# Performance work log

Hardware: AMD Instinct MI355X
Metric: run time of the kernel (lower is better)

## Reference

```python
import jax, jax.numpy as jnp
import numpy as np

N = 100000      # nodes
E = 1600000     # edges
H = 4           # num_heads
D = 16          # hidden_size per head
F_IN = 128      # input_size
HD = H * D
EPS = 1e-5


def setup_inputs() -> dict:
    key = jax.random.key(0)
    ks = jax.random.split(key, 12)
    s = 1.0 / np.sqrt(F_IN)
    feature = jax.random.normal(ks[0], (N, F_IN), jnp.float32)
    src = jax.random.randint(ks[1], (E,), 0, N, jnp.int32)
    dst = jax.random.randint(ks[2], (E,), 0, N, jnp.int32)
    Wq = jax.random.normal(ks[3], (F_IN, HD), jnp.float32) * s
    bq = jnp.zeros((HD,), jnp.float32)
    Wk = jax.random.normal(ks[4], (F_IN, HD), jnp.float32) * s
    bk = jnp.zeros((HD,), jnp.float32)
    Wv = jax.random.normal(ks[5], (F_IN, HD), jnp.float32) * s
    bv = jnp.zeros((HD,), jnp.float32)
    Wskip = jax.random.normal(ks[6], (F_IN, HD), jnp.float32) * s
    bskip = jnp.zeros((HD,), jnp.float32)
    ln_g = jnp.ones((HD,), jnp.float32)
    ln_b = jnp.zeros((HD,), jnp.float32)
    return dict(feature=feature, src=src, dst=dst, Wq=Wq, bq=bq, Wk=Wk, bk=bk,
                Wv=Wv, bv=bv, Wskip=Wskip, bskip=bskip, ln_g=ln_g, ln_b=ln_b)


def reference(feature, src, dst, Wq, bq, Wk, bk, Wv, bv, Wskip, bskip, ln_g, ln_b):
    # QKV projections, [N, H, D]; q scaled by 1/sqrt(D) (as in send_recv)
    q = ((feature @ Wq) + bq).reshape(N, H, D) * (1.0 / np.sqrt(D))
    k = ((feature @ Wk) + bk).reshape(N, H, D)
    v = ((feature @ Wv) + bv).reshape(N, H, D)
    # edge scores: sum over head dim of q[dst] * k[src] -> [E, H]
    alpha = jnp.sum(q[dst] * k[src], axis=-1)
    # segment softmax over incoming edges of each destination node
    m = jax.ops.segment_max(alpha, dst, num_segments=N)          # [N, H]
    ex = jnp.exp(alpha - m[dst])                                 # [E, H]
    z = jax.ops.segment_sum(ex, dst, num_segments=N)             # [N, H]
    a = ex / z[dst]                                              # [E, H]
    # weighted values, concat heads, scatter-sum to destination nodes
    msg = (v[src] * a[:, :, None]).reshape(E, HD)                # [E, H*D]
    out = jax.ops.segment_sum(msg, dst, num_segments=N)          # [N, H*D]
    # skip connection (no gate)
    out = out + (feature @ Wskip) + bskip
    # layer norm over last dim
    mu = jnp.mean(out, axis=-1, keepdims=True)
    var = jnp.mean(jnp.square(out - mu), axis=-1, keepdims=True)
    out = (out - mu) * jax.lax.rsqrt(var + EPS) * ln_g + ln_b
    return out
```

## Files before the change

kernel.cpp:

```cpp
#include <hip/hip_runtime.h>

typedef unsigned short u16;
typedef __attribute__((ext_vector_type(8))) short short8;
typedef __attribute__((ext_vector_type(4))) float f32x4;

#define N_NODES 100000
#define N_EDGES 1600000
#define F_IN    128
#define HD      64
#define LN_EPS  1e-5f

#define HIST_BLOCKS  6250
#define PROJ_BLOCKS  1563
#define SCAT_BLOCKS  6250
#define SCAN_BLOCKS  98

__device__ u16 g_WT[4 * HD * F_IN];

__device__ __forceinline__ float bf2f(u16 u) {
    union { unsigned int i; float f; } x;
    x.i = ((unsigned int)u) << 16;
    return x.f;
}
__device__ __forceinline__ u16 f2bf(float f) {
    unsigned int u;
    __builtin_memcpy(&u, &f, 4);
    unsigned int r = u + 0x7FFFu + ((u >> 16) & 1u);
    return (u16)(r >> 16);
}
__device__ __forceinline__ void ld4m(const void* p, int idx, int mode, float o[4]) {
    if (mode) {
        const float4 v = *reinterpret_cast<const float4*>((const float*)p + idx);
        o[0] = v.x; o[1] = v.y; o[2] = v.z; o[3] = v.w;
    } else {
        const ushort4 v = *reinterpret_cast<const ushort4*>((const u16*)p + idx);
        o[0] = bf2f(v.x); o[1] = bf2f(v.y); o[2] = bf2f(v.z); o[3] = bf2f(v.w);
    }
}

__global__ __launch_bounds__(256) void fused1_r13(
    const int* __restrict__ dst, int* __restrict__ deg,
    const void* __restrict__ Wq, const void* __restrict__ Wk,
    const void* __restrict__ Wv, const void* __restrict__ Ws,
    const u16* __restrict__ feat, int* __restrict__ mode)
{
    const int bid = blockIdx.x;
    if (bid < 16) {
        const int m  = bid >> 2;
        const int kg = bid & 3;
        const u16* W = (const u16*)((m == 0) ? Wq : (m == 1) ? Wk
                                  : (m == 2) ? Wv : Ws);
        const int t  = threadIdx.x;
        const int k  = kg * 32 + (t >> 3);
        const int c0 = (t & 7) * 8;
        union { uint4 v; u16 s[8]; } row;
        row.v = *reinterpret_cast<const uint4*>(W + k * HD + c0);
        u16* outp = g_WT + m * HD * F_IN;
        #pragma unroll
        for (int j = 0; j < 8; ++j)
            outp[(c0 + j) * F_IN + k] = row.s[j];
    } else if (bid == 16) {
        const int lane = threadIdx.x;
        if (lane < 64) {
            float mx = 0.f;
            #pragma unroll
            for (int i = 0; i < 4; ++i)
                mx = fmaxf(mx, fabsf(bf2f(feat[lane * 4 + i])));
            #pragma unroll
            for (int o = 1; o < 64; o <<= 1) mx = fmaxf(mx, __shfl_xor(mx, o));
            if (lane == 0) *mode = (mx > 1000.f) ? 1 : 0;
        }
    } else {
        const int e = (bid - 17) * 256 + threadIdx.x;
        if (e < N_EDGES) atomicAdd(&deg[dst[e]], 1);
    }
}

__global__ __launch_bounds__(1024) void scanA_r13(const int* __restrict__ deg,
                                                  int* __restrict__ off,
                                                  int* __restrict__ bsum)
{
    __shared__ int wsum[16];
    __shared__ int wexcl[16];
    const int tid = threadIdx.x, lane = tid & 63, wid = tid >> 6;
    const int idx = blockIdx.x * 1024 + tid;
    const int v = (idx < N_NODES) ? deg[idx] : 0;
    int sc = v;
    #pragma unroll
    for (int o = 1; o < 64; o <<= 1) {
        int t = __shfl_up(sc, o);
        if (lane >= o) sc += t;
    }
    if (lane == 63) wsum[wid] = sc;
    __syncthreads();
    if (tid == 0) {
        int run = 0;
        for (int i = 0; i < 16; ++i) { wexcl[i] = run; run += wsum[i]; }
        bsum[blockIdx.x] = run;
    }
    __syncthreads();
    if (idx < N_NODES) off[idx] = wexcl[wid] + (sc - v);
}

__global__ __launch_bounds__(1024) void scanC_r13(const int* __restrict__ deg,
                                                  int* __restrict__ off,
                                                  int* __restrict__ woff,
                                                  const int* __restrict__ bsum)
{
    __shared__ int base_s;
    const int tid = threadIdx.x;
    const int bid = blockIdx.x;
    if (tid == 0) {
        int run = 0;
        for (int i = 0; i < bid; ++i) run += bsum[i];
        base_s = run;
    }
    __syncthreads();
    const int base = base_s;
    const int idx = bid * 1024 + tid;
    if (idx < N_NODES) {
        const int e = off[idx] + base;
        off[idx]  = e;
        woff[idx] = e;
        if (idx == N_NODES - 1) off[N_NODES] = e + deg[idx];
    }
}

__global__ __launch_bounds__(256) void fused2_r13(
    const void* __restrict__ feature,
    const void* __restrict__ Wq, const void* __restrict__ bq,
    const void* __restrict__ Wk, const void* __restrict__ bk,
    const void* __restrict__ Wv, const void* __restrict__ bv,
    const void* __restrict__ Ws, const void* __restrict__ bs,
    u16* __restrict__ Qb, unsigned int* __restrict__ KV, u16* __restrict__ Sb,
    const int* __restrict__ mode_p,
    const int* __restrict__ src, const int* __restrict__ dst,
    int* __restrict__ woff, int* __restrict__ srcs)
{
    __shared__ u16 lq[16 * 64];
    __shared__ u16 lk[16 * 64];
    __shared__ u16 lv[16 * 64];
    __shared__ u16 ls[16 * 64];

    const int bid = blockIdx.x;

    if (bid % 5 != 0) {
        const int sid = bid - bid / 5 - 1;
        const int e = sid * 256 + threadIdx.x;
        if (e < N_EDGES) {
            const int d = dst[e];
            const int pos = atomicAdd(&woff[d], 1);
            srcs[pos] = src[e];
        }
        return;
    }

    const int pid  = bid / 5;
    const int mode = *mode_p;
    const int tid  = threadIdx.x;
    const int w    = tid >> 6;
    const int lane = tid & 63;

    const void* W;
    const void* b;
    float scale = 1.0f;
    if      (w == 0) { W = Wq; b = bq; scale = 0.25f; }
    else if (w == 1) { W = Wk; b = bk; }
    else if (w == 2) { W = Wv; b = bv; }
    else             { W = Ws; b = bs; }

    if (mode == 0) {
        const u16* F = (const u16*)feature;
        const int h = lane >> 4;
        const int c = lane & 15;

        const u16* WT = g_WT + w * HD * F_IN;
        short8 wfrag[4][4];
        #pragma unroll
        for (int ct = 0; ct < 4; ++ct) {
            const int col = ct * 16 + c;
            #pragma unroll
            for (int ks = 0; ks < 4; ++ks)
                wfrag[ct][ks] = *reinterpret_cast<const short8*>(
                    WT + col * F_IN + ks * 32 + h * 8);
        }

        float bias_f[4][4];
        #pragma unroll
        for (int ct = 0; ct < 4; ++ct) {
            const ushort4 bu =
                *reinterpret_cast<const ushort4*>((const u16*)b + ct * 16 + h * 4);
            bias_f[ct][0] = bf2f(bu.x); bias_f[ct][1] = bf2f(bu.y);
            bias_f[ct][2] = bf2f(bu.z); bias_f[ct][3] = bf2f(bu.w);
        }

        u16* Lmine = (w == 0) ? lq : (w == 1) ? lk : (w == 2) ? lv : ls;

        short8 fr[2][4];
        {
            const size_t arow = (size_t)(pid * 64 + c) * F_IN;
            #pragma unroll
            for (int ks = 0; ks < 4; ++ks)
                fr[0][ks] = *reinterpret_cast<const short8*>(F + arow + ks * 32 + h * 8);
        }

        #pragma unroll
        for (int t = 0; t < 4; ++t) {
            const int nbase = pid * 64 + t * 16;
            if (nbase >= N_NODES) break;
            const int cur = t & 1, nxt = cur ^ 1;

            const int nb2 = nbase + 16;
            if (t < 3 && nb2 < N_NODES) {
                const size_t arow = (size_t)(nb2 + c) * F_IN;
                #pragma unroll
                for (int ks = 0; ks < 4; ++ks)
                    fr[nxt][ks] =
                        *reinterpret_cast<const short8*>(F + arow + ks * 32 + h * 8);
            }

            f32x4 acc[4];
            #pragma unroll
            for (int ct = 0; ct < 4; ++ct) acc[ct] = (f32x4){0.f, 0.f, 0.f, 0.f};
            #pragma unroll
            for (int ks = 0; ks < 4; ++ks)
                #pragma unroll
                for (int ct = 0; ct < 4; ++ct)
                    acc[ct] = __builtin_amdgcn_mfma_f32_16x16x32_bf16(
                        wfrag[ct][ks], fr[cur][ks], acc[ct], 0, 0, 0);

            #pragma unroll
            for (int ct = 0; ct < 4; ++ct) {
                ushort4 pk;
                pk.x = f2bf((acc[ct][0] + bias_f[ct][0]) * scale);
                pk.y = f2bf((acc[ct][1] + bias_f[ct][1]) * scale);
                pk.z = f2bf((acc[ct][2] + bias_f[ct][2]) * scale);
                pk.w = f2bf((acc[ct][3] + bias_f[ct][3]) * scale);
                const int bo = (ct * 32 + h * 8) ^ ((c & 7) << 4);
                *reinterpret_cast<ushort4*>(
                    reinterpret_cast<char*>(Lmine) + c * 128 + bo) = pk;
            }
            __syncthreads();

            {
                const int half = tid >> 7;
                const int tt   = tid & 127;
                const int row  = tt >> 3, seg = tt & 7;
                const int ro   = (seg * 16) ^ ((row & 7) << 4);
                const uint4 qs = *reinterpret_cast<const uint4*>(
                    reinterpret_cast<const char*>(half ? ls : lq) + row * 128 + ro);
                *reinterpret_cast<uint4*>(
                    (half ? Sb : Qb) + (size_t)(nbase + row) * HD + seg * 8) = qs;

                const int krow = tid >> 4, c4 = tid & 15;
                const int ko   = (c4 * 8) ^ ((krow & 7) << 4);
                const ushort4 kk = *reinterpret_cast<const ushort4*>(
                    reinterpret_cast<const char*>(lk) + krow * 128 + ko);
                const ushort4 vv = *reinterpret_cast<const ushort4*>(
                    reinterpret_cast<const char*>(lv) + krow * 128 + ko);
                uint4 o;
                o.x = (unsigned)kk.x | ((unsigned)vv.x << 16);
                o.y = (unsigned)kk.y | ((unsigned)vv.y << 16);
                o.z = (unsigned)kk.z | ((unsigned)vv.z << 16);
                o.w = (unsigned)kk.w | ((unsigned)vv.w << 16);
                *reinterpret_cast<uint4*>(
                    KV + (size_t)(nbase + krow) * HD + c4 * 4) = o;
            }
            __syncthreads();
        }
    } else {
        const int colg  = lane & 15;
        const int nodeg = lane >> 4;
        const int c0    = colg * 4;
        const int kvsub = (w == 1) ? 0 : 1;
        u16* KVu = (u16*)KV;

        for (int st = 0; st < 4; ++st) {
            if (pid * 64 + st * 16 >= N_NODES) break;
            const int node_base = pid * 64 + st * 16 + nodeg * 4;

            float acc[4][4];
            #pragma unroll
            for (int n = 0; n < 4; ++n)
                #pragma unroll
                for (int cc = 0; cc < 4; ++cc) acc[n][cc] = 0.f;

            for (int k = 0; k < F_IN; k += 4) {
                float wv4[4][4];
                #pragma unroll
                for (int kk = 0; kk < 4; ++kk)
                    ld4m(W, (k + kk) * HD + c0, 1, wv4[kk]);
                #pragma unroll
                for (int n = 0; n < 4; ++n) {
                    float f[4];
                    ld4m(feature, (node_base + n) * F_IN + k, 1, f);
                    #pragma unroll
                    for (int cc = 0; cc < 4; ++cc)
                        acc[n][cc] += f[0] * wv4[0][cc] + f[1] * wv4[1][cc]
                                    + f[2] * wv4[2][cc] + f[3] * wv4[3][cc];
                }
            }

            float bias[4];
            ld4m(b, c0, 1, bias);

            #pragma unroll
            for (int n = 0; n < 4; ++n) {
                const int node = node_base + n;
                u16 r[4];
                #pragma unroll
                for (int cc = 0; cc < 4; ++cc)
                    r[cc] = f2bf((acc[n][cc] + bias[cc]) * scale);

                if (w == 0 || w == 3) {
                    u16* O = (w == 0) ? Qb : Sb;
                    ushort4 u4; u4.x = r[0]; u4.y = r[1]; u4.z = r[2]; u4.w = r[3];
                    *reinterpret_cast<ushort4*>(O + (size_t)node * HD + c0) = u4;
                } else {
                    #pragma unroll
                    for (int cc = 0; cc < 4; ++cc)
                        KVu[(size_t)node * 2 * HD + 2 * (c0 + cc) + kvsub] = r[cc];
                }
            }
        }
    }
}

__global__ __launch_bounds__(256) void attn_r13(
    const u16* __restrict__ Qb, const unsigned int* __restrict__ KV,
    const u16* __restrict__ Sb,
    const int* __restrict__ off, const int* __restrict__ srcs,
    const void* __restrict__ ln_g, const void* __restrict__ ln_b,
    void* __restrict__ out, const int* __restrict__ mode_p)
{
    const int mode = *mode_p;
    const int node = blockIdx.x * 4 + (threadIdx.x >> 6);
    const int lane = threadIdx.x & 63;

    const float qv = bf2f(Qb[(size_t)node * HD + lane]);
    const int e0 = off[node], e1 = off[node + 1];

    float z = 0.f, acc = 0.f;
    for (int base = e0; base < e1; base += 64) {
        const int n_e = min(64, e1 - base);
        int sidx = (base + lane < e1) ? srcs[base + lane] : 0;
        sidx = (sidx < 0) ? 0 : ((sidx >= N_NODES) ? N_NODES - 1 : sidx);
        int i = 0;
        for (; i + 4 <= n_e; i += 4) {
            const int s0 = __shfl(sidx, i);
            const int s1 = __shfl(sidx, i + 1);
            const int s2 = __shfl(sidx, i + 2);
            const int s3 = __shfl(sidx, i + 3);
            const unsigned int kv0 = KV[(size_t)s0 * HD + lane];
            const unsigned int kv1 = KV[(size_t)s1 * HD + lane];
            const unsigned int kv2 = KV[(size_t)s2 * HD + lane];
            const unsigned int kv3 = KV[(size_t)s3 * HD + lane];
            float p0 = qv * bf2f((u16)(kv0 & 0xffffu));
            float p1 = qv * bf2f((u16)(kv1 & 0xffffu));
            float p2 = qv * bf2f((u16)(kv2 & 0xffffu));
            float p3 = qv * bf2f((u16)(kv3 & 0xffffu));
            #pragma unroll
            for (int m = 1; m < 16; m <<= 1) {
                p0 += __shfl_xor(p0, m);
                p1 += __shfl_xor(p1, m);
                p2 += __shfl_xor(p2, m);
                p3 += __shfl_xor(p3, m);
            }
            const float x0 = __expf(p0);
            const float x1 = __expf(p1);
            const float x2 = __expf(p2);
            const float x3 = __expf(p3);
            z   += (x0 + x1) + (x2 + x3);
            acc += x0 * bf2f((u16)(kv0 >> 16)) + x1 * bf2f((u16)(kv1 >> 16))
                 + x2 * bf2f((u16)(kv2 >> 16)) + x3 * bf2f((u16)(kv3 >> 16));
        }
        for (; i < n_e; ++i) {
            const int s = __shfl(sidx, i);
            const unsigned int kv = KV[(size_t)s * HD + lane];
            float p = qv * bf2f((u16)(kv & 0xffffu));
            #pragma unroll
            for (int m = 1; m < 16; m <<= 1) p += __shfl_xor(p, m);
            const float ex = __expf(p);
            z   += ex;
            acc += ex * bf2f((u16)(kv >> 16));
        }
    }

    const float msg = (e1 > e0) ? (acc / z) : 0.f;
    float t = msg + bf2f(Sb[(size_t)node * HD + lane]);

    float mu = t;
    #pragma unroll
    for (int m = 1; m < 64; m <<= 1) mu += __shfl_xor(mu, m);
    mu *= (1.f / 64.f);
    const float d = t - mu;
    float var = d * d;
    #pragma unroll
    for (int m = 1; m < 64; m <<= 1) var += __shfl_xor(var, m);
    var *= (1.f / 64.f);
    const float r = d * rsqrtf(var + LN_EPS);

    const float g  = mode ? ((const float*)ln_g)[lane] : bf2f(((const u16*)ln_g)[lane]);
    const float bb = mode ? ((const float*)ln_b)[lane] : bf2f(((const u16*)ln_b)[lane]);
    const float res = r * g + bb;
    const size_t o = (size_t)node * HD + lane;
    if (mode) ((float*)out)[o] = res;
    else      ((u16*)out)[o]   = f2bf(res);
}

extern "C" void kernel_launch(void* const* d_in, const int* in_sizes, int n_in,
                              void* d_out, int out_size, void* d_ws, size_t ws_size,
                              hipStream_t stream)
{
    const void* feature = d_in[0];
    const int*  src     = (const int*)d_in[1];
    const int*  dst     = (const int*)d_in[2];
    const void* Wq = d_in[3];  const void* bq = d_in[4];
    const void* Wk = d_in[5];  const void* bk = d_in[6];
    const void* Wv = d_in[7];  const void* bv = d_in[8];
    const void* Ws = d_in[9];  const void* bs = d_in[10];
    const void* ln_g = d_in[11];
    const void* ln_b = d_in[12];

    u16* Qb = (u16*)d_ws;
    unsigned int* KV = (unsigned int*)(Qb + (size_t)N_NODES * HD);
    u16* Sb = (u16*)(KV + (size_t)N_NODES * HD);
    int* deg  = (int*)(Sb + (size_t)N_NODES * HD);
    int* off  = deg + N_NODES;
    int* woff = off + (N_NODES + 1);
    int* srcs = woff + N_NODES;
    int* mode = srcs + N_EDGES;
    int* bsum = mode + 1;

    const size_t need = (size_t)((char*)(bsum + SCAN_BLOCKS) - (char*)d_ws);
    if (ws_size < need) return;

    hipMemsetAsync(deg, 0, N_NODES * sizeof(int), stream);

    fused1_r13<<<dim3(17 + HIST_BLOCKS), dim3(256), 0, stream>>>(
        dst, deg, Wq, Wk, Wv, Ws, (const u16*)feature, mode);

    scanA_r13<<<dim3(SCAN_BLOCKS), dim3(1024), 0, stream>>>(deg, off, bsum);
    scanC_r13<<<dim3(SCAN_BLOCKS), dim3(1024), 0, stream>>>(deg, off, woff, bsum);

    fused2_r13<<<dim3(PROJ_BLOCKS + SCAT_BLOCKS), dim3(256), 0, stream>>>(
        feature, Wq, bq, Wk, bk, Wv, bv, Ws, bs,
        Qb, KV, Sb, mode, src, dst, woff, srcs);

    attn_r13<<<dim3(N_NODES / 4), dim3(256), 0, stream>>>(
        Qb, KV, Sb, off, srcs, ln_g, ln_b, d_out, mode);
}
```

Baseline: 555.4 us.

## Split projection across histogram and scatter phases, unroll attention gather by eight

```diff
diff --git a/kernel.cpp b/kernel.cpp
--- a/kernel.cpp
+++ b/kernel.cpp
@@ -10,10 +10,12 @@
 #define HD      64
 #define LN_EPS  1e-5f
 
-#define HIST_BLOCKS  6250
-#define PROJ_BLOCKS  1563
-#define SCAT_BLOCKS  6250
 #define SCAN_BLOCKS  98
+#define PROJ_TOTAL   1563
+#define PROJ_A       625
+#define PH1_GRID     6875
+#define PROJ_B       938
+#define PH2_GRID     7504
 
 __device__ u16 g_WT[4 * HD * F_IN];
 
@@ -28,18 +30,189 @@
     unsigned int r = u + 0x7FFFu + ((u >> 16) & 1u);
     return (u16)(r >> 16);
 }
-__device__ __forceinline__ void ld4m(const void* p, int idx, int mode, float o[4]) {
-    if (mode) {
-        const float4 v = *reinterpret_cast<const float4*>((const float*)p + idx);
-        o[0] = v.x; o[1] = v.y; o[2] = v.z; o[3] = v.w;
+__device__ __forceinline__ void ld4m(const void* p, int idx, float o[4]) {
+    const float4 v = *reinterpret_cast<const float4*>((const float*)p + idx);
+    o[0] = v.x; o[1] = v.y; o[2] = v.z; o[3] = v.w;
+}
+
+__device__ __forceinline__ void proj_body(
+    int pid, int mode,
+    const void* feature,
+    const void* Wq, const void* bq, const void* Wk, const void* bk,
+    const void* Wv, const void* bv, const void* Ws, const void* bs,
+    u16* Qb, unsigned int* KV, u16* Sb,
+    u16* lq, u16* lk, u16* lv, u16* ls)
+{
+    const int tid  = threadIdx.x;
+    const int w    = tid >> 6;
+    const int lane = tid & 63;
+
+    const void* W;
+    const void* b;
+    float scale = 1.0f;
+    if      (w == 0) { W = Wq; b = bq; scale = 0.25f; }
+    else if (w == 1) { W = Wk; b = bk; }
+    else if (w == 2) { W = Wv; b = bv; }
+    else             { W = Ws; b = bs; }
+
+    if (mode == 0) {
+        const u16* F = (const u16*)feature;
+        const int h = lane >> 4;
+        const int c = lane & 15;
+
+        const u16* WT = g_WT + w * HD * F_IN;
+        short8 wfrag[4][4];
+        #pragma unroll
+        for (int ct = 0; ct < 4; ++ct) {
+            const int col = ct * 16 + c;
+            #pragma unroll
+            for (int ks = 0; ks < 4; ++ks)
+                wfrag[ct][ks] = *reinterpret_cast<const short8*>(
+                    WT + col * F_IN + ks * 32 + h * 8);
+        }
+
+        float bias_f[4][4];
+        #pragma unroll
+        for (int ct = 0; ct < 4; ++ct) {
+            const ushort4 bu =
+                *reinterpret_cast<const ushort4*>((const u16*)b + ct * 16 + h * 4);
+            bias_f[ct][0] = bf2f(bu.x); bias_f[ct][1] = bf2f(bu.y);
+            bias_f[ct][2] = bf2f(bu.z); bias_f[ct][3] = bf2f(bu.w);
+        }
+
+        u16* Lmine = (w == 0) ? lq : (w == 1) ? lk : (w == 2) ? lv : ls;
+
+        short8 fr[2][4];
+        {
+            const size_t arow = (size_t)(pid * 64 + c) * F_IN;
+            #pragma unroll
+            for (int ks = 0; ks < 4; ++ks)
+                fr[0][ks] = *reinterpret_cast<const short8*>(F + arow + ks * 32 + h * 8);
+        }
+
+        #pragma unroll
+        for (int t = 0; t < 4; ++t) {
+            const int nbase = pid * 64 + t * 16;
+            if (nbase >= N_NODES) break;
+            const int cur = t & 1, nxt = cur ^ 1;
+
+            const int nb2 = nbase + 16;
+            if (t < 3 && nb2 < N_NODES) {
+                const size_t arow = (size_t)(nb2 + c) * F_IN;
+                #pragma unroll
+                for (int ks = 0; ks < 4; ++ks)
+                    fr[nxt][ks] =
+                        *reinterpret_cast<const short8*>(F + arow + ks * 32 + h * 8);
+            }
+
+            f32x4 acc[4];
+            #pragma unroll
+            for (int ct = 0; ct < 4; ++ct) acc[ct] = (f32x4){0.f, 0.f, 0.f, 0.f};
+            #pragma unroll
+            for (int ks = 0; ks < 4; ++ks)
+                #pragma unroll
+                for (int ct = 0; ct < 4; ++ct)
+                    acc[ct] = __builtin_amdgcn_mfma_f32_16x16x32_bf16(
+                        wfrag[ct][ks], fr[cur][ks], acc[ct], 0, 0, 0);
+
+            #pragma unroll
+            for (int ct = 0; ct < 4; ++ct) {
+                ushort4 pk;
+                pk.x = f2bf((acc[ct][0] + bias_f[ct][0]) * scale);
+                pk.y = f2bf((acc[ct][1] + bias_f[ct][1]) * scale);
+                pk.z = f2bf((acc[ct][2] + bias_f[ct][2]) * scale);
+                pk.w = f2bf((acc[ct][3] + bias_f[ct][3]) * scale);
+                const int bo = (ct * 32 + h * 8) ^ ((c & 7) << 4);
+                *reinterpret_cast<ushort4*>(
+                    reinterpret_cast<char*>(Lmine) + c * 128 + bo) = pk;
+            }
+            __syncthreads();
+
+            {
+                const int half = tid >> 7;
+                const int tt   = tid & 127;
+                const int row  = tt >> 3, seg = tt & 7;
+                const int ro   = (seg * 16) ^ ((row & 7) << 4);
+                const uint4 qs = *reinterpret_cast<const uint4*>(
+                    reinterpret_cast<const char*>(half ? ls : lq) + row * 128 + ro);
+                *reinterpret_cast<uint4*>(
+                    (half ? Sb : Qb) + (size_t)(nbase + row) * HD + seg * 8) = qs;
+
+                const int krow = tid >> 4, c4 = tid & 15;
+                const int ko   = (c4 * 8) ^ ((krow & 7) << 4);
+                const ushort4 kk = *reinterpret_cast<const ushort4*>(
+                    reinterpret_cast<const char*>(lk) + krow * 128 + ko);
+                const ushort4 vv = *reinterpret_cast<const ushort4*>(
+                    reinterpret_cast<const char*>(lv) + krow * 128 + ko);
+                uint4 o;
+                o.x = (unsigned)kk.x | ((unsigned)vv.x << 16);
+                o.y = (unsigned)kk.y | ((unsigned)vv.y << 16);
+                o.z = (unsigned)kk.z | ((unsigned)vv.z << 16);
+                o.w = (unsigned)kk.w | ((unsigned)vv.w << 16);
+                *reinterpret_cast<uint4*>(
+                    KV + (size_t)(nbase + krow) * HD + c4 * 4) = o;
+            }
+            __syncthreads();
+        }
     } else {
-        const ushort4 v = *reinterpret_cast<const ushort4*>((const u16*)p + idx);
-        o[0] = bf2f(v.x); o[1] = bf2f(v.y); o[2] = bf2f(v.z); o[3] = bf2f(v.w);
-    }
-}
-
-__global__ __launch_bounds__(256) void fused1_r13(
-    const int* __restrict__ dst, int* __restrict__ deg,
+        const int colg  = lane & 15;
+        const int nodeg = lane >> 4;
+        const int c0    = colg * 4;
+        const int kvsub = (w == 1) ? 0 : 1;
+        u16* KVu = (u16*)KV;
+
+        for (int st = 0; st < 4; ++st) {
+            if (pid * 64 + st * 16 >= N_NODES) break;
+            const int node_base = pid * 64 + st * 16 + nodeg * 4;
+
+            float acc[4][4];
+            #pragma unroll
+            for (int n = 0; n < 4; ++n)
+                #pragma unroll
+                for (int cc = 0; cc < 4; ++cc) acc[n][cc] = 0.f;
+
+            for (int k = 0; k < F_IN; k += 4) {
+                float wv4[4][4];
+                #pragma unroll
+                for (int kk = 0; kk < 4; ++kk)
+                    ld4m(W, (k + kk) * HD + c0, wv4[kk]);
+                #pragma unroll
+                for (int n = 0; n < 4; ++n) {
+                    float f[4];
+                    ld4m(feature, (node_base + n) * F_IN + k, f);
+                    #pragma unroll
+                    for (int cc = 0; cc < 4; ++cc)
+                        acc[n][cc] += f[0] * wv4[0][cc] + f[1] * wv4[1][cc]
+                                    + f[2] * wv4[2][cc] + f[3] * wv4[3][cc];
+                }
+            }
+
+            float bias[4];
+            ld4m(b, c0, bias);
+
+            #pragma unroll
+            for (int n = 0; n < 4; ++n) {
+                const int node = node_base + n;
+                u16 r[4];
+                #pragma unroll
+                for (int cc = 0; cc < 4; ++cc)
+                    r[cc] = f2bf((acc[n][cc] + bias[cc]) * scale);
+
+                if (w == 0 || w == 3) {
+                    u16* O = (w == 0) ? Qb : Sb;
+                    ushort4 u4; u4.x = r[0]; u4.y = r[1]; u4.z = r[2]; u4.w = r[3];
+                    *reinterpret_cast<ushort4*>(O + (size_t)node * HD + c0) = u4;
+                } else {
+                    #pragma unroll
+                    for (int cc = 0; cc < 4; ++cc)
+                        KVu[(size_t)node * 2 * HD + 2 * (c0 + cc) + kvsub] = r[cc];
+                }
+            }
+        }
+    }
+}
+
+__global__ __launch_bounds__(256) void tiny0_r14(
     const void* __restrict__ Wq, const void* __restrict__ Wk,
     const void* __restrict__ Wv, const void* __restrict__ Ws,
     const u16* __restrict__ feat, int* __restrict__ mode)
@@ -59,7 +232,7 @@
         #pragma unroll
         for (int j = 0; j < 8; ++j)
             outp[(c0 + j) * F_IN + k] = row.s[j];
-    } else if (bid == 16) {
+    } else {
         const int lane = threadIdx.x;
         if (lane < 64) {
             float mx = 0.f;
@@ -70,13 +243,36 @@
             for (int o = 1; o < 64; o <<= 1) mx = fmaxf(mx, __shfl_xor(mx, o));
             if (lane == 0) *mode = (mx > 1000.f) ? 1 : 0;
         }
-    } else {
-        const int e = (bid - 17) * 256 + threadIdx.x;
+    }
+}
+
+__global__ __launch_bounds__(256) void ph1_r14(
+    const void* __restrict__ feature,
+    const void* __restrict__ Wq, const void* __restrict__ bq,
+    const void* __restrict__ Wk, const void* __restrict__ bk,
+    const void* __restrict__ Wv, const void* __restrict__ bv,
+    const void* __restrict__ Ws, const void* __restrict__ bs,
+    u16* __restrict__ Qb, unsigned int* __restrict__ KV, u16* __restrict__ Sb,
+    const int* __restrict__ mode_p,
+    const int* __restrict__ dst, int* __restrict__ deg)
+{
+    __shared__ u16 lq[16 * 64];
+    __shared__ u16 lk[16 * 64];
+    __shared__ u16 lv[16 * 64];
+    __shared__ u16 ls[16 * 64];
+
+    const int bid = blockIdx.x;
+    if (bid % 11 != 0) {
+        const int hid = bid - bid / 11 - 1;
+        const int e = hid * 256 + threadIdx.x;
         if (e < N_EDGES) atomicAdd(&deg[dst[e]], 1);
-    }
-}
-
-__global__ __launch_bounds__(1024) void scanA_r13(const int* __restrict__ deg,
+        return;
+    }
+    proj_body(bid / 11, *mode_p, feature, Wq, bq, Wk, bk, Wv, bv, Ws, bs,
+              Qb, KV, Sb, lq, lk, lv, ls);
+}
+
+__global__ __launch_bounds__(1024) void scanA_r14(const int* __restrict__ deg,
                                                   int* __restrict__ off,
                                                   int* __restrict__ bsum)
 {
@@ -102,7 +298,7 @@
     if (idx < N_NODES) off[idx] = wexcl[wid] + (sc - v);
 }
 
-__global__ __launch_bounds__(1024) void scanC_r13(const int* __restrict__ deg,
+__global__ __launch_bounds__(1024) void scanC_r14(const int* __restrict__ deg,
                                                   int* __restrict__ off,
                                                   int* __restrict__ woff,
                                                   const int* __restrict__ bsum)
@@ -126,7 +322,7 @@
     }
 }
 
-__global__ __launch_bounds__(256) void fused2_r13(
+__global__ __launch_bounds__(256) void ph2_r14(
     const void* __restrict__ feature,
     const void* __restrict__ Wq, const void* __restrict__ bq,
     const void* __restrict__ Wk, const void* __restrict__ bk,
@@ -143,9 +339,8 @@
     __shared__ u16 ls[16 * 64];
 
     const int bid = blockIdx.x;
-
-    if (bid % 5 != 0) {
-        const int sid = bid - bid / 5 - 1;
+    if (bid % 8 != 0) {
+        const int sid = bid - bid / 8 - 1;
         const int e = sid * 256 + threadIdx.x;
         if (e < N_EDGES) {
             const int d = dst[e];
@@ -154,179 +349,11 @@
         }
         return;
     }
-
-    const int pid  = bid / 5;
-    const int mode = *mode_p;
-    const int tid  = threadIdx.x;
-    const int w    = tid >> 6;
-    const int lane = tid & 63;
-
-    const void* W;
-    const void* b;
-    float scale = 1.0f;
-    if      (w == 0) { W = Wq; b = bq; scale = 0.25f; }
-    else if (w == 1) { W = Wk; b = bk; }
-    else if (w == 2) { W = Wv; b = bv; }
-    else             { W = Ws; b = bs; }
-
-    if (mode == 0) {
-        const u16* F = (const u16*)feature;
-        const int h = lane >> 4;
-        const int c = lane & 15;
-
-        const u16* WT = g_WT + w * HD * F_IN;
-        short8 wfrag[4][4];
-        #pragma unroll
-        for (int ct = 0; ct < 4; ++ct) {
-            const int col = ct * 16 + c;
-            #pragma unroll
-            for (int ks = 0; ks < 4; ++ks)
-                wfrag[ct][ks] = *reinterpret_cast<const short8*>(
-                    WT + col * F_IN + ks * 32 + h * 8);
-        }
-
-        float bias_f[4][4];
-        #pragma unroll
-        for (int ct = 0; ct < 4; ++ct) {
-            const ushort4 bu =
-                *reinterpret_cast<const ushort4*>((const u16*)b + ct * 16 + h * 4);
-            bias_f[ct][0] = bf2f(bu.x); bias_f[ct][1] = bf2f(bu.y);
-            bias_f[ct][2] = bf2f(bu.z); bias_f[ct][3] = bf2f(bu.w);
-        }
-
-        u16* Lmine = (w == 0) ? lq : (w == 1) ? lk : (w == 2) ? lv : ls;
-
-        short8 fr[2][4];
-        {
-            const size_t arow = (size_t)(pid * 64 + c) * F_IN;
-            #pragma unroll
-            for (int ks = 0; ks < 4; ++ks)
-                fr[0][ks] = *reinterpret_cast<const short8*>(F + arow + ks * 32 + h * 8);
-        }
-
-        #pragma unroll
-        for (int t = 0; t < 4; ++t) {
-            const int nbase = pid * 64 + t * 16;
-            if (nbase >= N_NODES) break;
-            const int cur = t & 1, nxt = cur ^ 1;
-
-            const int nb2 = nbase + 16;
-            if (t < 3 && nb2 < N_NODES) {
-                const size_t arow = (size_t)(nb2 + c) * F_IN;
-                #pragma unroll
-                for (int ks = 0; ks < 4; ++ks)
-                    fr[nxt][ks] =
-                        *reinterpret_cast<const short8*>(F + arow + ks * 32 + h * 8);
-            }
-
-            f32x4 acc[4];
-            #pragma unroll
-            for (int ct = 0; ct < 4; ++ct) acc[ct] = (f32x4){0.f, 0.f, 0.f, 0.f};
-            #pragma unroll
-            for (int ks = 0; ks < 4; ++ks)
-                #pragma unroll
-                for (int ct = 0; ct < 4; ++ct)
-                    acc[ct] = __builtin_amdgcn_mfma_f32_16x16x32_bf16(
-                        wfrag[ct][ks], fr[cur][ks], acc[ct], 0, 0, 0);
-
-            #pragma unroll
-            for (int ct = 0; ct < 4; ++ct) {
-                ushort4 pk;
-                pk.x = f2bf((acc[ct][0] + bias_f[ct][0]) * scale);
-                pk.y = f2bf((acc[ct][1] + bias_f[ct][1]) * scale);
-                pk.z = f2bf((acc[ct][2] + bias_f[ct][2]) * scale);
-                pk.w = f2bf((acc[ct][3] + bias_f[ct][3]) * scale);
-                const int bo = (ct * 32 + h * 8) ^ ((c & 7) << 4);
-                *reinterpret_cast<ushort4*>(
-                    reinterpret_cast<char*>(Lmine) + c * 128 + bo) = pk;
-            }
-            __syncthreads();
-
-            {
-                const int half = tid >> 7;
-                const int tt   = tid & 127;
-                const int row  = tt >> 3, seg = tt & 7;
-                const int ro   = (seg * 16) ^ ((row & 7) << 4);
-                const uint4 qs = *reinterpret_cast<const uint4*>(
-                    reinterpret_cast<const char*>(half ? ls : lq) + row * 128 + ro);
-                *reinterpret_cast<uint4*>(
-                    (half ? Sb : Qb) + (size_t)(nbase + row) * HD + seg * 8) = qs;
-
-                const int krow = tid >> 4, c4 = tid & 15;
-                const int ko   = (c4 * 8) ^ ((krow & 7) << 4);
-                const ushort4 kk = *reinterpret_cast<const ushort4*>(
-                    reinterpret_cast<const char*>(lk) + krow * 128 + ko);
-                const ushort4 vv = *reinterpret_cast<const ushort4*>(
-                    reinterpret_cast<const char*>(lv) + krow * 128 + ko);
-                uint4 o;
-                o.x = (unsigned)kk.x | ((unsigned)vv.x << 16);
-                o.y = (unsigned)kk.y | ((unsigned)vv.y << 16);
-                o.z = (unsigned)kk.z | ((unsigned)vv.z << 16);
-                o.w = (unsigned)kk.w | ((unsigned)vv.w << 16);
-                *reinterpret_cast<uint4*>(
-                    KV + (size_t)(nbase + krow) * HD + c4 * 4) = o;
-            }
-            __syncthreads();
-        }
-    } else {
-        const int colg  = lane & 15;
-        const int nodeg = lane >> 4;
-        const int c0    = colg * 4;
-        const int kvsub = (w == 1) ? 0 : 1;
-        u16* KVu = (u16*)KV;
-
-        for (int st = 0; st < 4; ++st) {
-            if (pid * 64 + st * 16 >= N_NODES) break;
-            const int node_base = pid * 64 + st * 16 + nodeg * 4;
-
-            float acc[4][4];
-            #pragma unroll
-            for (int n = 0; n < 4; ++n)
-                #pragma unroll
-                for (int cc = 0; cc < 4; ++cc) acc[n][cc] = 0.f;
-
-            for (int k = 0; k < F_IN; k += 4) {
-                float wv4[4][4];
-                #pragma unroll
-                for (int kk = 0; kk < 4; ++kk)
-                    ld4m(W, (k + kk) * HD + c0, 1, wv4[kk]);
-                #pragma unroll
-                for (int n = 0; n < 4; ++n) {
-                    float f[4];
-                    ld4m(feature, (node_base + n) * F_IN + k, 1, f);
-                    #pragma unroll
-                    for (int cc = 0; cc < 4; ++cc)
-                        acc[n][cc] += f[0] * wv4[0][cc] + f[1] * wv4[1][cc]
-                                    + f[2] * wv4[2][cc] + f[3] * wv4[3][cc];
-                }
-            }
-
-            float bias[4];
-            ld4m(b, c0, 1, bias);
-
-            #pragma unroll
-            for (int n = 0; n < 4; ++n) {
-                const int node = node_base + n;
-                u16 r[4];
-                #pragma unroll
-                for (int cc = 0; cc < 4; ++cc)
-                    r[cc] = f2bf((acc[n][cc] + bias[cc]) * scale);
-
-                if (w == 0 || w == 3) {
-                    u16* O = (w == 0) ? Qb : Sb;
-                    ushort4 u4; u4.x = r[0]; u4.y = r[1]; u4.z = r[2]; u4.w = r[3];
-                    *reinterpret_cast<ushort4*>(O + (size_t)node * HD + c0) = u4;
-                } else {
-                    #pragma unroll
-                    for (int cc = 0; cc < 4; ++cc)
-                        KVu[(size_t)node * 2 * HD + 2 * (c0 + cc) + kvsub] = r[cc];
-                }
-            }
-        }
-    }
-}
-
-__global__ __launch_bounds__(256) void attn_r13(
+    proj_body(PROJ_A + bid / 8, *mode_p, feature, Wq, bq, Wk, bk, Wv, bv, Ws, bs,
+              Qb, KV, Sb, lq, lk, lv, ls);
+}
+
+__global__ __launch_bounds__(256) void attn_r14(
     const u16* __restrict__ Qb, const unsigned int* __restrict__ KV,
     const u16* __restrict__ Sb,
     const int* __restrict__ off, const int* __restrict__ srcs,
@@ -346,33 +373,53 @@
         int sidx = (base + lane < e1) ? srcs[base + lane] : 0;
         sidx = (sidx < 0) ? 0 : ((sidx >= N_NODES) ? N_NODES - 1 : sidx);
         int i = 0;
+        for (; i + 8 <= n_e; i += 8) {
+            unsigned int kv[8];
+            float p[8];
+            #pragma unroll
+            for (int j = 0; j < 8; ++j) {
+                const int s = __shfl(sidx, i + j);
+                kv[j] = KV[(size_t)s * HD + lane];
+            }
+            #pragma unroll
+            for (int j = 0; j < 8; ++j)
+                p[j] = qv * bf2f((u16)(kv[j] & 0xffffu));
+            #pragma unroll
+            for (int m = 1; m < 16; m <<= 1) {
+                #pragma unroll
+                for (int j = 0; j < 8; ++j) p[j] += __shfl_xor(p[j], m);
+            }
+            float zp = 0.f, ap = 0.f;
+            #pragma unroll
+            for (int j = 0; j < 8; ++j) {
+                const float x = __expf(p[j]);
+                zp += x;
+                ap += x * bf2f((u16)(kv[j] >> 16));
+            }
+            z += zp; acc += ap;
+        }
         for (; i + 4 <= n_e; i += 4) {
-            const int s0 = __shfl(sidx, i);
-            const int s1 = __shfl(sidx, i + 1);
-            const int s2 = __shfl(sidx, i + 2);
-            const int s3 = __shfl(sidx, i + 3);
-            const unsigned int kv0 = KV[(size_t)s0 * HD + lane];
-            const unsigned int kv1 = KV[(size_t)s1 * HD + lane];
-            const unsigned int kv2 = KV[(size_t)s2 * HD + lane];
-            const unsigned int kv3 = KV[(size_t)s3 * HD + lane];
-            float p0 = qv * bf2f((u16)(kv0 & 0xffffu));
-            float p1 = qv * bf2f((u16)(kv1 & 0xffffu));
-            float p2 = qv * bf2f((u16)(kv2 & 0xffffu));
-            float p3 = qv * bf2f((u16)(kv3 & 0xffffu));
+            unsigned int kv[4];
+            float p[4];
+            #pragma unroll
+            for (int j = 0; j < 4; ++j) {
+                const int s = __shfl(sidx, i + j);
+                kv[j] = KV[(size_t)s * HD + lane];
+            }
+            #pragma unroll
+            for (int j = 0; j < 4; ++j)
+                p[j] = qv * bf2f((u16)(kv[j] & 0xffffu));
             #pragma unroll
             for (int m = 1; m < 16; m <<= 1) {
-                p0 += __shfl_xor(p0, m);
-                p1 += __shfl_xor(p1, m);
-                p2 += __shfl_xor(p2, m);
-                p3 += __shfl_xor(p3, m);
-            }
-            const float x0 = __expf(p0);
-            const float x1 = __expf(p1);
-            const float x2 = __expf(p2);
-            const float x3 = __expf(p3);
-            z   += (x0 + x1) + (x2 + x3);
-            acc += x0 * bf2f((u16)(kv0 >> 16)) + x1 * bf2f((u16)(kv1 >> 16))
-                 + x2 * bf2f((u16)(kv2 >> 16)) + x3 * bf2f((u16)(kv3 >> 16));
+                #pragma unroll
+                for (int j = 0; j < 4; ++j) p[j] += __shfl_xor(p[j], m);
+            }
+            #pragma unroll
+            for (int j = 0; j < 4; ++j) {
+                const float x = __expf(p[j]);
+                z   += x;
+                acc += x * bf2f((u16)(kv[j] >> 16));
+            }
         }
         for (; i < n_e; ++i) {
             const int s = __shfl(sidx, i);
@@ -437,16 +484,20 @@
 
     hipMemsetAsync(deg, 0, N_NODES * sizeof(int), stream);
 
-    fused1_r13<<<dim3(17 + HIST_BLOCKS), dim3(256), 0, stream>>>(
-        dst, deg, Wq, Wk, Wv, Ws, (const u16*)feature, mode);
-
-    scanA_r13<<<dim3(SCAN_BLOCKS), dim3(1024), 0, stream>>>(deg, off, bsum);
-    scanC_r13<<<dim3(SCAN_BLOCKS), dim3(1024), 0, stream>>>(deg, off, woff, bsum);
-
-    fused2_r13<<<dim3(PROJ_BLOCKS + SCAT_BLOCKS), dim3(256), 0, stream>>>(
+    tiny0_r14<<<dim3(17), dim3(256), 0, stream>>>(
+        Wq, Wk, Wv, Ws, (const u16*)feature, mode);
+
+    ph1_r14<<<dim3(PH1_GRID), dim3(256), 0, stream>>>(
+        feature, Wq, bq, Wk, bk, Wv, bv, Ws, bs,
+        Qb, KV, Sb, mode, dst, deg);
+
+    scanA_r14<<<dim3(SCAN_BLOCKS), dim3(1024), 0, stream>>>(deg, off, bsum);
+    scanC_r14<<<dim3(SCAN_BLOCKS), dim3(1024), 0, stream>>>(deg, off, woff, bsum);
+
+    ph2_r14<<<dim3(PH2_GRID), dim3(256), 0, stream>>>(
         feature, Wq, bq, Wk, bk, Wv, bv, Ws, bs,
         Qb, KV, Sb, mode, src, dst, woff, srcs);
 
-    attn_r13<<<dim3(N_NODES / 4), dim3(256), 0, stream>>>(
+    attn_r14<<<dim3(N_NODES / 4), dim3(256), 0, stream>>>(
         Qb, KV, Sb, off, srcs, ln_g, ln_b, d_out, mode);
 }
```

Result: slower. 1.316 ms (+137.0%).
